# Kernel optimization log

Measured on AMD Instinct MI355X. Metric: run time of the kernel, lower is better.

## Reference

```python
import jax, jax.numpy as jnp
import numpy as np

N = 100000      # num nodes
E = 1600000     # num edges
NFEAT = 512
NHID = 256
NCLASS = 32
K = 10
ALPHA = 0.1


def setup_inputs() -> dict:
    key = jax.random.key(0)
    ks = jax.random.split(key, 6)
    x = jax.random.normal(ks[0], (N, NFEAT), dtype=jnp.float32)
    edge_index = jax.random.randint(ks[1], (2, E), 0, N, dtype=jnp.int32)
    edge_attr = jax.random.uniform(ks[2], (E,), dtype=jnp.float32)
    # Linear params (Kaiming-ish scale)
    W_start = jax.random.normal(ks[3], (NFEAT, NHID), dtype=jnp.float32) * np.float32(1.0 / np.sqrt(NFEAT))
    b_start = jnp.zeros((NHID,), jnp.float32)
    W_end = jax.random.normal(ks[4], (NHID, NCLASS), dtype=jnp.float32) * np.float32(1.0 / np.sqrt(NHID))
    b_end = jnp.zeros((NCLASS,), jnp.float32)
    # GPR 'PPR' init coefficients: temp[k] = alpha*(1-alpha)^k, temp[K] = (1-alpha)^K
    temp = (ALPHA * (1.0 - ALPHA) ** np.arange(K + 1)).astype(np.float32)
    temp[-1] = np.float32((1.0 - ALPHA) ** K)
    temp = jnp.asarray(temp)
    return {"x": x, "edge_attr": edge_attr, "W_start": W_start, "b_start": b_start,
            "W_end": W_end, "b_end": b_end, "temp": temp, "edge_index": edge_index}


def gcn_norm(edge_index, edge_weight, num_nodes):
    # add self loops with weight 1 (PyG default fill_value=1)
    loop = jnp.arange(num_nodes, dtype=edge_index.dtype)
    ei = jnp.concatenate([edge_index, jnp.stack([loop, loop])], axis=1)   # [2, E+N]
    ew = jnp.concatenate([edge_weight, jnp.ones((num_nodes,), edge_weight.dtype)])
    row, col = ei[0], ei[1]
    deg = jax.ops.segment_sum(ew, col, num_segments=num_nodes)            # [N]
    dis = jnp.where(deg > 0, jax.lax.rsqrt(jnp.where(deg > 0, deg, 1.0)), 0.0)
    norm = dis[row] * ew * dis[col]                                       # [E+N]
    return ei, norm


def reference(x, edge_attr, W_start, b_start, W_end, b_end, temp, edge_index):
    # MLP front-end (eval mode: dropout is identity)
    h = jax.nn.relu(x @ W_start + b_start)        # [N, NHID]
    h = jax.nn.relu(h @ W_end + b_end)            # [N, NCLASS]
    ei, norm = gcn_norm(edge_index, edge_attr, N)
    row, col = ei[0], ei[1]
    hidden = h * temp[0]
    xk = h
    for k in range(K):
        # SpMM: gather messages norm * x[row], scatter-add at col
        xk = jax.ops.segment_sum(norm[:, None] * xk[row], col, num_segments=N)
        hidden = hidden + temp[k + 1] * xk
    return hidden
```

## Files before the change

kernel.cpp:

```cpp
#include <hip/hip_runtime.h>

typedef __attribute__((ext_vector_type(8))) short short8;
typedef __attribute__((ext_vector_type(4))) float f32x4;
typedef unsigned long long u64;

constexpr int NN = 100000;
constexpr int EE = 1600000;
constexpr int NF = 512;
constexpr int NH = 256;
constexpr int NC = 32;
constexpr int KP = 10;

__device__ __forceinline__ unsigned short f2bf(float f) {
  unsigned int u = __float_as_uint(f);
  u += 0x7FFFu + ((u >> 16) & 1u);
  return (unsigned short)(u >> 16);
}
__device__ __forceinline__ float bf2f(unsigned short s) {
  return __uint_as_float(((unsigned int)s) << 16);
}
__device__ __forceinline__ int padc(int c) { return (c + 7) & ~7; }

__device__ __forceinline__ short8 cvt8(float4 a0, float4 a1) {
  union { unsigned int u[4]; short8 s; } r;
  asm("v_cvt_pk_bf16_f32 %0, %1, %2" : "=v"(r.u[0]) : "v"(a0.x), "v"(a0.y));
  asm("v_cvt_pk_bf16_f32 %0, %1, %2" : "=v"(r.u[1]) : "v"(a0.z), "v"(a0.w));
  asm("v_cvt_pk_bf16_f32 %0, %1, %2" : "=v"(r.u[2]) : "v"(a1.x), "v"(a1.y));
  asm("v_cvt_pk_bf16_f32 %0, %1, %2" : "=v"(r.u[3]) : "v"(a1.z), "v"(a1.w));
  return r.s;
}

__device__ __forceinline__ void block_sync_lds() {
  asm volatile("s_waitcnt lgkmcnt(0)" ::: "memory");
  __builtin_amdgcn_s_barrier();
}

__global__ void convwb_kernel(const float* __restrict__ Ws, const float* __restrict__ We,
                              unsigned short* __restrict__ Wt, unsigned short* __restrict__ Web) {
  int idx = blockIdx.x * 256 + threadIdx.x;
  if (idx < 131072) {
    int col = idx >> 9, k = idx & 511;
    Wt[idx] = f2bf(Ws[(size_t)k * NH + col]);
  } else {
    int j = idx - 131072;
    int col = j >> 8, k = j & 255;
    Web[j] = f2bf(We[(size_t)k * NC + col]);
  }
}

__global__ __launch_bounds__(256, 3) void gemm1_kernel(
    const float* __restrict__ X, const unsigned short* __restrict__ Wt,
    const float* __restrict__ bias, const unsigned short* __restrict__ Web,
    const float* __restrict__ be, const float* __restrict__ temp,
    unsigned short* __restrict__ x0b, float* __restrict__ out) {
  constexpr int PAD = 36;
  __shared__ __align__(16) unsigned short Asm[2][64 * PAD];
  __shared__ __align__(16) unsigned short Bsm[2][256 * PAD];
  const int tid = threadIdx.x;
  const int lane = tid & 63;
  const int w = tid >> 6;
  const int l15 = lane & 15, kq = lane >> 4;
  const int m0 = blockIdx.x * 64;

  const int arl = tid >> 2, aq = tid & 3;
  int ar = m0 + arl; if (ar >= NN) ar = NN - 1;
  const float* aptr = X + (size_t)ar * NF + aq * 8;
  const int awr = arl * PAD + aq * 8;
  const unsigned short* bptr = Wt + (size_t)tid * NF;
  const int bwr = tid * PAD;

  f32x4 acc[4][4];
#pragma unroll
  for (int m = 0; m < 4; m++)
#pragma unroll
    for (int n = 0; n < 4; n++) acc[m][n] = (f32x4)0.0f;

  float4 ra[3][2]; short8 rb[3][4];

#define LOADR(ks, j) do { \
    ra[j][0] = *reinterpret_cast<const float4*>(aptr + (ks) * 32); \
    ra[j][1] = *reinterpret_cast<const float4*>(aptr + (ks) * 32 + 4); \
    rb[j][0] = *reinterpret_cast<const short8*>(bptr + (ks) * 32); \
    rb[j][1] = *reinterpret_cast<const short8*>(bptr + (ks) * 32 + 8); \
    rb[j][2] = *reinterpret_cast<const short8*>(bptr + (ks) * 32 + 16); \
    rb[j][3] = *reinterpret_cast<const short8*>(bptr + (ks) * 32 + 24); \
  } while (0)

#define STAGE(b, j) do { \
    *reinterpret_cast<short8*>(&Asm[b][awr]) = cvt8(ra[j][0], ra[j][1]); \
    *reinterpret_cast<short8*>(&Bsm[b][bwr]) = rb[j][0]; \
    *reinterpret_cast<short8*>(&Bsm[b][bwr + 8]) = rb[j][1]; \
    *reinterpret_cast<short8*>(&Bsm[b][bwr + 16]) = rb[j][2]; \
    *reinterpret_cast<short8*>(&Bsm[b][bwr + 24]) = rb[j][3]; \
  } while (0)

#define COMPUTE(b) do { \
    short8 af[4], bfr[4]; \
    _Pragma("unroll") \
    for (int mi = 0; mi < 4; mi++) \
      af[mi] = *reinterpret_cast<const short8*>(&Asm[b][(mi * 16 + l15) * PAD + kq * 8]); \
    _Pragma("unroll") \
    for (int ni = 0; ni < 4; ni++) \
      bfr[ni] = *reinterpret_cast<const short8*>(&Bsm[b][(w * 64 + ni * 16 + l15) * PAD + kq * 8]); \
    _Pragma("unroll") \
    for (int mi = 0; mi < 4; mi++) \
      _Pragma("unroll") \
      for (int ni = 0; ni < 4; ni++) \
        acc[mi][ni] = __builtin_amdgcn_mfma_f32_16x16x32_bf16(af[mi], bfr[ni], acc[mi][ni], 0, 0, 0); \
  } while (0)

  LOADR(0, 0);
  LOADR(1, 1);
  LOADR(2, 2);
  STAGE(0, 0);
  block_sync_lds();

#pragma unroll
  for (int p = 0; p < 16; p++) {
    if (p + 3 < 16) LOADR(p + 3, (p + 3) % 3);
    COMPUTE(p & 1);
    if (p + 1 < 16) STAGE((p + 1) & 1, (p + 1) % 3);
    block_sync_lds();
  }
#undef LOADR
#undef STAGE
#undef COMPUTE

  unsigned short* Ht = (unsigned short*)Bsm;
  f32x4 acc2[2];
  acc2[0] = (f32x4)0.0f; acc2[1] = (f32x4)0.0f;
  const unsigned short* wrow = Web + (size_t)l15 * 256 + kq * 8;
#pragma unroll
  for (int p2 = 0; p2 < 2; p2++) {
    block_sync_lds();
    if ((w >> 1) == p2) {
#pragma unroll
      for (int ni = 0; ni < 4; ni++) {
        const int colg = w * 64 + ni * 16 + l15;
        const float bsv = bias[colg];
        const int cl = colg - p2 * 128;
#pragma unroll
        for (int mi = 0; mi < 4; mi++)
#pragma unroll
          for (int i = 0; i < 4; i++) {
            const int row = mi * 16 + kq * 4 + i;
            const float v = acc[mi][ni][i] + bsv;
            Ht[row * 136 + cl] = f2bf(v > 0.f ? v : 0.f);
          }
      }
    }
    block_sync_lds();
    const unsigned short* hr = Ht + (size_t)(w * 16 + l15) * 136 + kq * 8;
#pragma unroll
    for (int ks = 0; ks < 4; ks++) {
      short8 a  = *reinterpret_cast<const short8*>(hr + ks * 32);
      short8 b0 = *reinterpret_cast<const short8*>(wrow + p2 * 128 + ks * 32);
      short8 b1 = *reinterpret_cast<const short8*>(wrow + 16 * 256 + p2 * 128 + ks * 32);
      acc2[0] = __builtin_amdgcn_mfma_f32_16x16x32_bf16(a, b0, acc2[0], 0, 0, 0);
      acc2[1] = __builtin_amdgcn_mfma_f32_16x16x32_bf16(a, b1, acc2[1], 0, 0, 0);
    }
  }
  const float t0 = temp[0];
#pragma unroll
  for (int nt = 0; nt < 2; nt++) {
    const int col = nt * 16 + l15;
    const float bv = be[col];
#pragma unroll
    for (int i = 0; i < 4; i++) {
      const int row = m0 + w * 16 + kq * 4 + i;
      if (row < NN) {
        float v = acc2[nt][i] + bv;
        v = v > 0.f ? v : 0.f;
        x0b[(size_t)row * NC + col] = f2bf(v);
        out[(size_t)row * NC + col] = t0 * v;
      }
    }
  }
}

__global__ void node_init_kernel(u64* dc) {
  int i = blockIdx.x * 256 + threadIdx.x;
  if (i < NN) dc[i] = (1ULL << 44) | (1ULL << 32);
}

__global__ void edge_deg_kernel(const int* __restrict__ ei, const float* __restrict__ ew,
                                u64* dc) {
  int e = blockIdx.x * 256 + threadIdx.x;
  if (e < EE) {
    int col = ei[EE + e];
    u64 v = (1ULL << 44) | (u64)((double)ew[e] * 4294967296.0);
    atomicAdd(&dc[col], v);
  }
}

__global__ void dis_kernel(const u64* __restrict__ dc, float* __restrict__ dis,
                           int* __restrict__ cnt) {
  int i = blockIdx.x * 256 + threadIdx.x;
  if (i < NN) {
    u64 v = dc[i];
    cnt[i] = (int)(v >> 44);
    float deg = (float)((double)(v & 0xFFFFFFFFFFFULL) * (1.0 / 4294967296.0));
    dis[i] = rsqrtf(deg);
  }
}

__global__ void scan1_kernel(const int* __restrict__ cnt, int* bsum) {
  __shared__ int ws[4];
  const int tid = threadIdx.x;
  int base = blockIdx.x * 1024 + tid * 4;
  int s = 0;
#pragma unroll
  for (int j = 0; j < 4; j++) { int i = base + j; if (i < NN) s += padc(cnt[i]); }
  for (int off = 32; off > 0; off >>= 1) s += __shfl_down(s, off);
  if ((tid & 63) == 0) ws[tid >> 6] = s;
  __syncthreads();
  if (tid == 0) bsum[blockIdx.x] = ws[0] + ws[1] + ws[2] + ws[3];
}

__global__ void scan2_kernel(const int* __restrict__ bsum, int* bofs, int* offs) {
  if (threadIdx.x == 0) {
    int run = 0;
    for (int i = 0; i < 98; i++) { bofs[i] = run; run += bsum[i]; }
    offs[NN] = run;
  }
}

__global__ void scan3_kernel(const int* __restrict__ cnt, const int* __restrict__ bofs,
                             int* offs, int* cursor) {
  __shared__ int wsum[4];
  const int tid = threadIdx.x;
  const int lane = tid & 63, wv = tid >> 6;
  int base = blockIdx.x * 1024 + tid * 4;
  int v[4]; int s = 0;
#pragma unroll
  for (int j = 0; j < 4; j++) { int i = base + j; v[j] = (i < NN) ? padc(cnt[i]) : 0; s += v[j]; }
  int incl = s;
  for (int off = 1; off < 64; off <<= 1) {
    int t = __shfl_up(incl, off);
    if (lane >= off) incl += t;
  }
  if (lane == 63) wsum[wv] = incl;
  __syncthreads();
  int woff = bofs[blockIdx.x];
  for (int w = 0; w < wv; w++) woff += wsum[w];
  int excl = woff + incl - s;
#pragma unroll
  for (int j = 0; j < 4; j++) {
    int i = base + j;
    if (i < NN) { offs[i] = excl; cursor[i] = excl; }
    excl += v[j];
  }
}

__global__ void fill_kernel(const int* __restrict__ ei, const float* __restrict__ ew,
                            const float* __restrict__ dis, int* cursor,
                            u64* __restrict__ pk) {
  int t = blockIdx.x * 256 + threadIdx.x;
  if (t < EE) {
    int r = ei[t], c = ei[EE + t];
    int slot = atomicAdd(&cursor[c], 1);
    unsigned int wb = __float_as_uint(dis[r] * ew[t] * dis[c]);
    pk[slot] = (u64)(unsigned int)r | ((u64)wb << 32);
  } else if (t < EE + NN) {
    int i = t - EE;
    int slot = atomicAdd(&cursor[i], 1);
    float d = dis[i];
    unsigned int wb = __float_as_uint(d * d);
    pk[slot] = (u64)(unsigned int)i | ((u64)wb << 32);
  }
}

__global__ void pad_kernel(const int* __restrict__ cursor, const int* __restrict__ offs,
                           u64* __restrict__ pk) {
  int i = blockIdx.x * 256 + threadIdx.x;
  if (i < NN) {
    int j = cursor[i], e = offs[i + 1];
    for (; j < e; j++) pk[j] = 0;
  }
}

__global__ __launch_bounds__(256) void spmm_kernel(
    const int* __restrict__ offs, const u64* __restrict__ pk,
    const unsigned short* __restrict__ xin, unsigned short* __restrict__ xout) {
  const int tid = threadIdx.x;
  const int node = blockIdx.x * 32 + (tid >> 3);
  const int fq = (tid & 7) * 4;
  const int s = offs[node], e = offs[node + 1];
  float a0 = 0.f, a1 = 0.f, a2 = 0.f, a3 = 0.f;
  for (int j = s; j < e; j += 8) {
    ulonglong2 p01 = *reinterpret_cast<const ulonglong2*>(pk + j);
    ulonglong2 p23 = *reinterpret_cast<const ulonglong2*>(pk + j + 2);
    ulonglong2 p45 = *reinterpret_cast<const ulonglong2*>(pk + j + 4);
    ulonglong2 p67 = *reinterpret_cast<const ulonglong2*>(pk + j + 6);
    const u64 p[8] = {p01.x, p01.y, p23.x, p23.y, p45.x, p45.y, p67.x, p67.y};
    u64 q[8];
#pragma unroll
    for (int i = 0; i < 8; i++)
      q[i] = *reinterpret_cast<const u64*>(xin + (size_t)(unsigned int)p[i] * NC + fq);
#pragma unroll
    for (int i = 0; i < 8; i++) {
      const float w = __uint_as_float((unsigned int)(p[i] >> 32));
      a0 += w * bf2f((unsigned short)(q[i]));
      a1 += w * bf2f((unsigned short)(q[i] >> 16));
      a2 += w * bf2f((unsigned short)(q[i] >> 32));
      a3 += w * bf2f((unsigned short)(q[i] >> 48));
    }
  }
  unsigned int lo, hi;
  asm("v_cvt_pk_bf16_f32 %0, %1, %2" : "=v"(lo) : "v"(a0), "v"(a1));
  asm("v_cvt_pk_bf16_f32 %0, %1, %2" : "=v"(hi) : "v"(a2), "v"(a3));
  *reinterpret_cast<u64*>(xout + (size_t)node * NC + fq) =
      (u64)lo | ((u64)hi << 32);
}

__global__ __launch_bounds__(256) void wsum_kernel(
    const unsigned short* __restrict__ S07,
    const unsigned short* __restrict__ S8, const unsigned short* __restrict__ S9,
    float* __restrict__ out, const float* __restrict__ temp) {
  int t8 = blockIdx.x * 256 + threadIdx.x;
  if (t8 >= NN * NC / 8) return;
  const size_t base = (size_t)t8 * 8;
  float s[8];
  float4 o0 = *reinterpret_cast<const float4*>(out + base);
  float4 o1 = *reinterpret_cast<const float4*>(out + base + 4);
  s[0] = o0.x; s[1] = o0.y; s[2] = o0.z; s[3] = o0.w;
  s[4] = o1.x; s[5] = o1.y; s[6] = o1.z; s[7] = o1.w;
#pragma unroll
  for (int k = 0; k < 8; k++) {
    const float tk = temp[k + 1];
    short8 v = *reinterpret_cast<const short8*>(S07 + (size_t)k * NN * NC + base);
#pragma unroll
    for (int t = 0; t < 8; t++) s[t] += tk * bf2f((unsigned short)v[t]);
  }
  {
    const float tk = temp[9];
    short8 v = *reinterpret_cast<const short8*>(S8 + base);
#pragma unroll
    for (int t = 0; t < 8; t++) s[t] += tk * bf2f((unsigned short)v[t]);
  }
  {
    const float tk = temp[10];
    short8 v = *reinterpret_cast<const short8*>(S9 + base);
#pragma unroll
    for (int t = 0; t < 8; t++) s[t] += tk * bf2f((unsigned short)v[t]);
  }
  *reinterpret_cast<float4*>(out + base) = make_float4(s[0], s[1], s[2], s[3]);
  *reinterpret_cast<float4*>(out + base + 4) = make_float4(s[4], s[5], s[6], s[7]);
}

extern "C" void kernel_launch(void* const* d_in, const int* in_sizes, int n_in,
                              void* d_out, int out_size, void* d_ws, size_t ws_size,
                              hipStream_t stream) {
  const float* X    = (const float*)d_in[0];
  const float* EA   = (const float*)d_in[1];
  const float* Ws   = (const float*)d_in[2];
  const float* bs   = (const float*)d_in[3];
  const float* We   = (const float*)d_in[4];
  const float* be   = (const float*)d_in[5];
  const float* temp = (const float*)d_in[6];
  const int*   ei   = (const int*)d_in[7];
  float* out = (float*)d_out;

  size_t off = 0;
  auto alloc = [&](size_t n) { void* p = (char*)d_ws + off; off += (n + 255) & ~(size_t)255; return p; };
  unsigned short* Wt  = (unsigned short*)alloc((size_t)NF * NH * 2);
  unsigned short* Web = (unsigned short*)alloc((size_t)NH * NC * 2);
  unsigned short* SL  = (unsigned short*)alloc((size_t)NN * NH * 2);
  unsigned short* x0b = (unsigned short*)alloc((size_t)NN * NC * 2);
  unsigned short* xk8 = (unsigned short*)alloc((size_t)NN * NC * 2);
  unsigned short* xk9 = (unsigned short*)alloc((size_t)NN * NC * 2);
  u64*   dc   = (u64*)alloc((size_t)NN * 8);
  float* dis  = (float*)alloc((size_t)NN * 4);
  int*   cnt  = (int*)alloc((size_t)NN * 4);
  int*   offs = (int*)alloc((size_t)(NN + 1) * 4);
  int*   cursor = (int*)alloc((size_t)NN * 4);
  int*   bsum = (int*)alloc(98 * 4);
  int*   bofs = (int*)alloc(98 * 4);
  u64*   pk   = (u64*)alloc((size_t)(EE + 8 * NN) * 8);

  convwb_kernel<<<544, 256, 0, stream>>>(Ws, We, Wt, Web);
  gemm1_kernel<<<1563, 256, 0, stream>>>(X, Wt, bs, Web, be, temp, x0b, out);

  node_init_kernel<<<391, 256, 0, stream>>>(dc);
  edge_deg_kernel<<<6250, 256, 0, stream>>>(ei, EA, dc);
  dis_kernel<<<391, 256, 0, stream>>>(dc, dis, cnt);
  scan1_kernel<<<98, 256, 0, stream>>>(cnt, bsum);
  scan2_kernel<<<1, 64, 0, stream>>>(bsum, bofs, offs);
  scan3_kernel<<<98, 256, 0, stream>>>(cnt, bofs, offs, cursor);
  fill_kernel<<<6641, 256, 0, stream>>>(ei, EA, dis, cursor, pk);
  pad_kernel<<<391, 256, 0, stream>>>(cursor, offs, pk);

  auto slice = [&](int k) -> unsigned short* {
    return (k < 8) ? SL + (size_t)k * NN * NC : (k == 8 ? xk8 : xk9);
  };
  const unsigned short* xin = x0b;
  for (int k = 0; k < KP; k++) {
    spmm_kernel<<<3125, 256, 0, stream>>>(offs, pk, xin, slice(k));
    xin = slice(k);
  }
  wsum_kernel<<<1563, 256, 0, stream>>>(SL, xk8, xk9, out, temp);
}
```

Baseline: 537.6 us.

## Fuse final SpMM with weighted sum, merge scan stages, pre-zero padding

The last propagation step is fused with the weighted-sum epilogue, so the final hop's result never goes to memory and one full pass over the slices is dropped. The scan2 kernel is folded into scan3, with each block summing the preceding block totals itself. The pad kernel is replaced by zeroing the whole packed edge array inside node_init. The weight transpose/convert now uses an LDS-tiled transpose with vector stores. Together these cut kernel launches and memory traffic, at the cost of zeroing the full packed array instead of only the padding slots.

```diff
diff --git a/kernel.cpp b/kernel.cpp
--- a/kernel.cpp
+++ b/kernel.cpp
@@ -10,6 +10,7 @@
 constexpr int NH = 256;
 constexpr int NC = 32;
 constexpr int KP = 10;
+constexpr int PKN = EE + 8 * NN;
 
 __device__ __forceinline__ unsigned short f2bf(float f) {
   unsigned int u = __float_as_uint(f);
@@ -37,14 +38,31 @@
 
 __global__ void convwb_kernel(const float* __restrict__ Ws, const float* __restrict__ We,
                               unsigned short* __restrict__ Wt, unsigned short* __restrict__ Web) {
-  int idx = blockIdx.x * 256 + threadIdx.x;
-  if (idx < 131072) {
-    int col = idx >> 9, k = idx & 511;
-    Wt[idx] = f2bf(Ws[(size_t)k * NH + col]);
+  if (blockIdx.x < 32) {
+    __shared__ float tile[64][65];
+    const int k0 = (blockIdx.x >> 2) * 64;
+    const int c0 = (blockIdx.x & 3) * 64;
+    const int t = threadIdx.x;
+    const int g = t >> 6, l = t & 63;
+#pragma unroll
+    for (int j = 0; j < 16; j++) {
+      const int row = g * 16 + j;
+      tile[row][l] = Ws[(size_t)(k0 + row) * NH + c0 + l];
+    }
+    __syncthreads();
+    const int col = t >> 2, ks = (t & 3) * 16;
+    union { unsigned short us[16]; short8 s8[2]; } st;
+#pragma unroll
+    for (int i = 0; i < 16; i++) st.us[i] = f2bf(tile[ks + i][col]);
+    unsigned short* dst = Wt + (size_t)(c0 + col) * NF + k0 + ks;
+    *reinterpret_cast<short8*>(dst) = st.s8[0];
+    *reinterpret_cast<short8*>(dst + 8) = st.s8[1];
   } else {
-    int j = idx - 131072;
-    int col = j >> 8, k = j & 255;
-    Web[j] = f2bf(We[(size_t)k * NC + col]);
+    const int t = threadIdx.x;
+    const int col = t & 31, kb = (t >> 5) * 32;
+#pragma unroll
+    for (int i = 0; i < 32; i++)
+      Web[(size_t)col * 256 + kb + i] = f2bf(We[(size_t)(kb + i) * NC + col]);
   }
 }
 
@@ -178,9 +196,10 @@
   }
 }
 
-__global__ void node_init_kernel(u64* dc) {
+__global__ void node_init_kernel(u64* dc, u64* pk) {
   int i = blockIdx.x * 256 + threadIdx.x;
   if (i < NN) dc[i] = (1ULL << 44) | (1ULL << 32);
+  for (int j = i; j < PKN; j += 391 * 256) pk[j] = 0;
 }
 
 __global__ void edge_deg_kernel(const int* __restrict__ ei, const float* __restrict__ ew,
@@ -217,19 +236,22 @@
   if (tid == 0) bsum[blockIdx.x] = ws[0] + ws[1] + ws[2] + ws[3];
 }
 
-__global__ void scan2_kernel(const int* __restrict__ bsum, int* bofs, int* offs) {
-  if (threadIdx.x == 0) {
-    int run = 0;
-    for (int i = 0; i < 98; i++) { bofs[i] = run; run += bsum[i]; }
-    offs[NN] = run;
-  }
-}
-
-__global__ void scan3_kernel(const int* __restrict__ cnt, const int* __restrict__ bofs,
+__global__ void scan3_kernel(const int* __restrict__ cnt, const int* __restrict__ bsum,
                              int* offs, int* cursor) {
   __shared__ int wsum[4];
+  __shared__ int bofs_s;
   const int tid = threadIdx.x;
   const int lane = tid & 63, wv = tid >> 6;
+  if (tid == 0) {
+    int run = 0;
+    for (int i = 0; i < (int)blockIdx.x; i++) run += bsum[i];
+    bofs_s = run;
+    if (blockIdx.x == 0) {
+      int tot = 0;
+      for (int i = 0; i < 98; i++) tot += bsum[i];
+      offs[NN] = tot;
+    }
+  }
   int base = blockIdx.x * 1024 + tid * 4;
   int v[4]; int s = 0;
 #pragma unroll
@@ -241,7 +263,7 @@
   }
   if (lane == 63) wsum[wv] = incl;
   __syncthreads();
-  int woff = bofs[blockIdx.x];
+  int woff = bofs_s;
   for (int w = 0; w < wv; w++) woff += wsum[w];
   int excl = woff + incl - s;
 #pragma unroll
@@ -270,15 +292,6 @@
   }
 }
 
-__global__ void pad_kernel(const int* __restrict__ cursor, const int* __restrict__ offs,
-                           u64* __restrict__ pk) {
-  int i = blockIdx.x * 256 + threadIdx.x;
-  if (i < NN) {
-    int j = cursor[i], e = offs[i + 1];
-    for (; j < e; j++) pk[j] = 0;
-  }
-}
-
 __global__ __launch_bounds__(256) void spmm_kernel(
     const int* __restrict__ offs, const u64* __restrict__ pk,
     const unsigned short* __restrict__ xin, unsigned short* __restrict__ xout) {
@@ -313,39 +326,58 @@
       (u64)lo | ((u64)hi << 32);
 }
 
-__global__ __launch_bounds__(256) void wsum_kernel(
-    const unsigned short* __restrict__ S07,
-    const unsigned short* __restrict__ S8, const unsigned short* __restrict__ S9,
+__global__ __launch_bounds__(256) void spmm_wsum_kernel(
+    const int* __restrict__ offs, const u64* __restrict__ pk,
+    const unsigned short* __restrict__ xin,
+    const unsigned short* __restrict__ SL,
     float* __restrict__ out, const float* __restrict__ temp) {
-  int t8 = blockIdx.x * 256 + threadIdx.x;
-  if (t8 >= NN * NC / 8) return;
-  const size_t base = (size_t)t8 * 8;
-  float s[8];
-  float4 o0 = *reinterpret_cast<const float4*>(out + base);
-  float4 o1 = *reinterpret_cast<const float4*>(out + base + 4);
-  s[0] = o0.x; s[1] = o0.y; s[2] = o0.z; s[3] = o0.w;
-  s[4] = o1.x; s[5] = o1.y; s[6] = o1.z; s[7] = o1.w;
+  const int tid = threadIdx.x;
+  const int node = blockIdx.x * 32 + (tid >> 3);
+  const int fq = (tid & 7) * 4;
+  const int s = offs[node], e = offs[node + 1];
+  float a0 = 0.f, a1 = 0.f, a2 = 0.f, a3 = 0.f;
+  for (int j = s; j < e; j += 8) {
+    ulonglong2 p01 = *reinterpret_cast<const ulonglong2*>(pk + j);
+    ulonglong2 p23 = *reinterpret_cast<const ulonglong2*>(pk + j + 2);
+    ulonglong2 p45 = *reinterpret_cast<const ulonglong2*>(pk + j + 4);
+    ulonglong2 p67 = *reinterpret_cast<const ulonglong2*>(pk + j + 6);
+    const u64 p[8] = {p01.x, p01.y, p23.x, p23.y, p45.x, p45.y, p67.x, p67.y};
+    u64 q[8];
+#pragma unroll
+    for (int i = 0; i < 8; i++)
+      q[i] = *reinterpret_cast<const u64*>(xin + (size_t)(unsigned int)p[i] * NC + fq);
+#pragma unroll
+    for (int i = 0; i < 8; i++) {
+      const float w = __uint_as_float((unsigned int)(p[i] >> 32));
+      a0 += w * bf2f((unsigned short)(q[i]));
+      a1 += w * bf2f((unsigned short)(q[i] >> 16));
+      a2 += w * bf2f((unsigned short)(q[i] >> 32));
+      a3 += w * bf2f((unsigned short)(q[i] >> 48));
+    }
+  }
+  const size_t ob = (size_t)node * NC + fq;
+  float4 o = *reinterpret_cast<const float4*>(out + ob);
+  const float t10 = temp[10];
+  float r0 = o.x + t10 * a0, r1 = o.y + t10 * a1;
+  float r2 = o.z + t10 * a2, r3 = o.w + t10 * a3;
 #pragma unroll
   for (int k = 0; k < 8; k++) {
     const float tk = temp[k + 1];
-    short8 v = *reinterpret_cast<const short8*>(S07 + (size_t)k * NN * NC + base);
-#pragma unroll
-    for (int t = 0; t < 8; t++) s[t] += tk * bf2f((unsigned short)v[t]);
+    u64 q = *reinterpret_cast<const u64*>(SL + (size_t)k * NN * NC + ob);
+    r0 += tk * bf2f((unsigned short)(q));
+    r1 += tk * bf2f((unsigned short)(q >> 16));
+    r2 += tk * bf2f((unsigned short)(q >> 32));
+    r3 += tk * bf2f((unsigned short)(q >> 48));
   }
   {
     const float tk = temp[9];
-    short8 v = *reinterpret_cast<const short8*>(S8 + base);
-#pragma unroll
-    for (int t = 0; t < 8; t++) s[t] += tk * bf2f((unsigned short)v[t]);
-  }
-  {
-    const float tk = temp[10];
-    short8 v = *reinterpret_cast<const short8*>(S9 + base);
-#pragma unroll
-    for (int t = 0; t < 8; t++) s[t] += tk * bf2f((unsigned short)v[t]);
-  }
-  *reinterpret_cast<float4*>(out + base) = make_float4(s[0], s[1], s[2], s[3]);
-  *reinterpret_cast<float4*>(out + base + 4) = make_float4(s[4], s[5], s[6], s[7]);
+    u64 q = *reinterpret_cast<const u64*>(xin + ob);
+    r0 += tk * bf2f((unsigned short)(q));
+    r1 += tk * bf2f((unsigned short)(q >> 16));
+    r2 += tk * bf2f((unsigned short)(q >> 32));
+    r3 += tk * bf2f((unsigned short)(q >> 48));
+  }
+  *reinterpret_cast<float4*>(out + ob) = make_float4(r0, r1, r2, r3);
 }
 
 extern "C" void kernel_launch(void* const* d_in, const int* in_sizes, int n_in,
@@ -368,35 +400,31 @@
   unsigned short* SL  = (unsigned short*)alloc((size_t)NN * NH * 2);
   unsigned short* x0b = (unsigned short*)alloc((size_t)NN * NC * 2);
   unsigned short* xk8 = (unsigned short*)alloc((size_t)NN * NC * 2);
-  unsigned short* xk9 = (unsigned short*)alloc((size_t)NN * NC * 2);
   u64*   dc   = (u64*)alloc((size_t)NN * 8);
   float* dis  = (float*)alloc((size_t)NN * 4);
   int*   cnt  = (int*)alloc((size_t)NN * 4);
   int*   offs = (int*)alloc((size_t)(NN + 1) * 4);
   int*   cursor = (int*)alloc((size_t)NN * 4);
   int*   bsum = (int*)alloc(98 * 4);
-  int*   bofs = (int*)alloc(98 * 4);
-  u64*   pk   = (u64*)alloc((size_t)(EE + 8 * NN) * 8);
-
-  convwb_kernel<<<544, 256, 0, stream>>>(Ws, We, Wt, Web);
+  u64*   pk   = (u64*)alloc((size_t)PKN * 8);
+
+  convwb_kernel<<<33, 256, 0, stream>>>(Ws, We, Wt, Web);
   gemm1_kernel<<<1563, 256, 0, stream>>>(X, Wt, bs, Web, be, temp, x0b, out);
 
-  node_init_kernel<<<391, 256, 0, stream>>>(dc);
+  node_init_kernel<<<391, 256, 0, stream>>>(dc, pk);
   edge_deg_kernel<<<6250, 256, 0, stream>>>(ei, EA, dc);
   dis_kernel<<<391, 256, 0, stream>>>(dc, dis, cnt);
   scan1_kernel<<<98, 256, 0, stream>>>(cnt, bsum);
-  scan2_kernel<<<1, 64, 0, stream>>>(bsum, bofs, offs);
-  scan3_kernel<<<98, 256, 0, stream>>>(cnt, bofs, offs, cursor);
+  scan3_kernel<<<98, 256, 0, stream>>>(cnt, bsum, offs, cursor);
   fill_kernel<<<6641, 256, 0, stream>>>(ei, EA, dis, cursor, pk);
-  pad_kernel<<<391, 256, 0, stream>>>(cursor, offs, pk);
 
   auto slice = [&](int k) -> unsigned short* {
-    return (k < 8) ? SL + (size_t)k * NN * NC : (k == 8 ? xk8 : xk9);
+    return (k < 8) ? SL + (size_t)k * NN * NC : xk8;
   };
   const unsigned short* xin = x0b;
-  for (int k = 0; k < KP; k++) {
+  for (int k = 0; k < KP - 1; k++) {
     spmm_kernel<<<3125, 256, 0, stream>>>(offs, pk, xin, slice(k));
     xin = slice(k);
   }
-  wsum_kernel<<<1563, 256, 0, stream>>>(SL, xk8, xk9, out, temp);
-}
+  spmm_wsum_kernel<<<3125, 256, 0, stream>>>(offs, pk, xk8, SL, out, temp);
+}
```

Result: no change. 534.6 us (-0.5%).
